# Kernel tuning notes

Hardware: AMD Instinct MI355X
Metric: run time of the kernel (lower is better)

The kernel has to match this reference:

```python
import jax, jax.numpy as jnp
import numpy as np
from jax import lax

DT = 0.1
V_DES = 12.64798288
T_HW = 0.50284384
A_MAX = 0.10033688
B_SAFE = 4.98937183
DELTA = 1.0
S0 = 0.13082412

B, S, I, H, K = 2048, 128, 8, 256, 50


def _lstm_layer(x, Wih, Whh, bih, bhh):
    # x: (B, S, in). PyTorch gate order: i, f, g, o. Fold both biases once.
    Bn = x.shape[0]
    Hd = Whh.shape[1]
    xg = jnp.einsum('bsi,gi->bsg', x, Wih) + bih + bhh  # (B, S, 4H)

    def step(carry, xg_t):
        h, c = carry
        g = xg_t + h @ Whh.T
        i, f, gg, o = jnp.split(g, 4, axis=-1)
        c = jax.nn.sigmoid(f) * c + jax.nn.sigmoid(i) * jnp.tanh(gg)
        h = jax.nn.sigmoid(o) * jnp.tanh(c)
        return (h, c), h

    init = (jnp.zeros((Bn, Hd), x.dtype), jnp.zeros((Bn, Hd), x.dtype))
    _, hs = lax.scan(step, init, jnp.swapaxes(xg, 0, 1))
    return jnp.swapaxes(hs, 0, 1)  # (B, S, H)


def _idm_rollout(v0, s_gap0, v_lead, horizon):
    sqrt_ab = float(np.sqrt(max(A_MAX, 1e-6) * max(B_SAFE, 1e-6)))

    def step(carry, _):
        v, s = carry
        dv = v_lead - v
        s_c = jnp.maximum(s, 1e-6)
        s_star = jnp.maximum(S0 + v * T_HW + v * dv / (2.0 * sqrt_ab + 1e-6), 0.0)
        acc = A_MAX * (1.0 - (v / V_DES) ** DELTA - (s_star / s_c) ** 2)
        v_next = jnp.maximum(v + DT * acc, 0.0)
        s_next = jnp.maximum(s + dv * DT, 1e-6)
        return (v_next, s_next), v_next

    _, vs = lax.scan(step, (v0, s_gap0), None, length=horizon)
    return jnp.swapaxes(vs, 0, 1)  # (B, K)


def setup_inputs() -> dict:
    key = jax.random.key(0)
    ks = jax.random.split(key, 14)
    sc = 0.05
    x = jax.random.uniform(ks[0], (B, S, I), jnp.float32) * 12.0  # speeds/features in [0, 12] m/s
    s_safe = 1.0 + jax.random.uniform(ks[1], (B,), jnp.float32) * 49.0  # gap in [1, 50] m
    v_lead = jax.random.uniform(ks[2], (B,), jnp.float32) * 12.0
    return {
        'x': x,
        's_safe_initial': s_safe,
        'v_lead_initial': v_lead,
        'Wih0': jax.random.normal(ks[3], (4 * H, I), jnp.float32) * sc,
        'Whh0': jax.random.normal(ks[4], (4 * H, H), jnp.float32) * sc,
        'bih0': jax.random.normal(ks[5], (4 * H,), jnp.float32) * sc,
        'bhh0': jax.random.normal(ks[6], (4 * H,), jnp.float32) * sc,
        'Wih1': jax.random.normal(ks[7], (4 * H, H), jnp.float32) * sc,
        'Whh1': jax.random.normal(ks[8], (4 * H, H), jnp.float32) * sc,
        'bih1': jax.random.normal(ks[9], (4 * H,), jnp.float32) * sc,
        'bhh1': jax.random.normal(ks[10], (4 * H,), jnp.float32) * sc,
        'Wfc': jax.random.normal(ks[11], (K, H), jnp.float32) * sc,
        'bfc': jax.random.normal(ks[12], (K,), jnp.float32) * sc,
    }


def reference(x, s_safe_initial, v_lead_initial, Wih0, Whh0, bih0, bhh0,
              Wih1, Whh1, bih1, bhh1, Wfc, bfc):
    h = _lstm_layer(x, Wih0, Whh0, bih0, bhh0)
    h = _lstm_layer(h, Wih1, Whh1, bih1, bhh1)
    y_lstm = h[:, -1, :] @ Wfc.T + bfc  # (B, K)
    y_idm = _idm_rollout(x[:, -1, 0], s_safe_initial, v_lead_initial, Wfc.shape[0])
    return (y_lstm, y_idm)
```

## Files before the change

kernel.cpp:

```cpp
#include <hip/hip_runtime.h>
#include <stdint.h>

typedef float f32x4 __attribute__((ext_vector_type(4)));
typedef unsigned int uint;
typedef unsigned long long ull;
typedef unsigned short ushort_t;

#define NB 2048
#define NS 128
#define NI 8
#define NH 256
#define NG 1024
#define NK 50

#define A_SC 16.0f
#define W_SC 32.0f
#define SC_PROD 512.0f
#define INV_SC (1.0f/(A_SC*W_SC))

#define DT_    0.1f
#define V_DES_ 12.64798288f
#define T_HW_  0.50284384f
#define A_MAX_ 0.10033688f
#define B_SAFE_ 4.98937183f
#define S0_    0.13082412f

#define HADDR(row, boff) (((row) << 8) + (((((boff) >> 3) ^ ((row) & 15)) & 31) << 3) + ((boff) & 7))
#define GIDX(row, col) (((row) << 7) + ((col) ^ (((row) & 12) << 2)))

__device__ __forceinline__ uint8_t f2fp8(float v) {
    int r = __builtin_amdgcn_cvt_pk_fp8_f32(v, v, 0, false);
    return (uint8_t)(r & 0xff);
}
__device__ __forceinline__ float sigm(float x) { return 1.0f / (1.0f + __expf(-x)); }
__device__ __forceinline__ float tanh_f(float x) {
    x = fminf(fmaxf(x, -15.0f), 15.0f);
    float e = __expf(2.0f * x);
    return (e - 1.0f) / (e + 1.0f);
}

__global__ void k_pack(const float* __restrict__ W, uint8_t* __restrict__ out,
                       int tiles, int KB, int Nsrc, int Ksrc) {
    int gid = blockIdx.x * 256 + threadIdx.x;
    int total = tiles * KB * 64;
    if (gid >= total) return;
    int lane = gid & 63;
    int kb   = (gid >> 6) % KB;
    int tile = gid / (64 * KB);
    int n = tile * 16 + (lane & 15);
    int kbase = kb * 32 + (lane >> 4) * 8;
    uint64_t wbits = 0;
    #pragma unroll
    for (int j = 0; j < 8; ++j) {
        int k = kbase + j;
        float v = (n < Nsrc && k < Ksrc) ? W[(size_t)n * Ksrc + k] * W_SC : 0.0f;
        wbits |= ((uint64_t)f2fp8(v)) << (8 * j);
    }
    *(uint64_t*)(out + (size_t)gid * 8) = wbits;
}

__global__ void k_bias(const float* __restrict__ bih0, const float* __restrict__ bhh0,
                       const float* __restrict__ bih1, const float* __restrict__ bhh1,
                       float* __restrict__ b0, float* __restrict__ b1) {
    int i = blockIdx.x * 256 + threadIdx.x;
    if (i < NG) b0[i] = (bih0[i] + bhh0[i]) * SC_PROD;
    else if (i < 2 * NG) b1[i - NG] = (bih1[i - NG] + bhh1[i - NG]) * SC_PROD;
}

__global__ void k_x8(const float* __restrict__ x, uint8_t* __restrict__ x8) {
    int i = blockIdx.x * 256 + threadIdx.x;
    if (i < NB * NS * NI) x8[i] = f2fp8(x[i] * A_SC);
}

__global__ __launch_bounds__(512, 4)
void k_lstm4(const uint8_t* __restrict__ x8,
             const uint8_t* __restrict__ Wih0P, const uint8_t* __restrict__ Whh0P,
             const uint8_t* __restrict__ Wih1P, const uint8_t* __restrict__ Whh1P,
             const uint8_t* __restrict__ WfcP,
             const float* __restrict__ bias0, const float* __restrict__ bias1,
             const float* __restrict__ bfc,
             uint8_t* __restrict__ h0g, uint8_t* __restrict__ h1g,
             uint* __restrict__ ctrs, float* __restrict__ out) {
    __shared__ uint8_t h0st[8192];
    __shared__ uint8_t h1st[8192];
    __shared__ float gA[4096];
    __shared__ float gB[4096];

    const int tid  = threadIdx.x;
    const int w    = tid >> 6, lane = tid & 63;
    const int lrow = lane & 15, kgrp = lane >> 4;
    const int blk  = blockIdx.x;
    const int grp  = blk >> 3, slc = blk & 7;
    const int rowbase = grp * 32;
    const int g = w & 3, uh = w >> 2;
    const int T = g * 16 + slc * 2 + uh;

    long wI0, wH0[8], wI1[8], wH1[8];
    wI0 = *(const long*)(Wih0P + ((size_t)T * 64 + lane) * 8);
    #pragma unroll
    for (int kb = 0; kb < 8; ++kb) {
        wH0[kb] = *(const long*)(Whh0P + (((size_t)T * 8 + kb) * 64 + lane) * 8);
        wI1[kb] = *(const long*)(Wih1P + (((size_t)T * 8 + kb) * 64 + lane) * 8);
        wH1[kb] = *(const long*)(Whh1P + (((size_t)T * 8 + kb) * 64 + lane) * 8);
    }
    asm volatile("" : "+v"(wI0));
    #pragma unroll
    for (int kb = 0; kb < 8; ++kb)
        asm volatile("" : "+v"(wH0[kb]), "+v"(wI1[kb]), "+v"(wH1[kb]));

    const int colw = g * 32 + uh * 16 + lrow;
    const float bw0 = bias0[g * 256 + slc * 32 + uh * 16 + lrow];
    const float bw1 = bias1[g * 256 + slc * 32 + uh * 16 + lrow];

    const int nrow = tid >> 4;
    const int nu2  = (tid & 15) * 2;
    float c0v[2] = {0, 0}, c1v[2] = {0, 0};

    { int4 z = {0,0,0,0}; ((int4*)h0st)[tid] = z; ((int4*)h1st)[tid] = z; }
    __syncthreads();

    const int abase = HADDR(lrow, kgrp * 8);
    uint8_t* const h0base = h0g + (size_t)grp * 16384;
    uint8_t* const h1base = h1g + (size_t)grp * 16384;
    uint* const myctr = ctrs + grp * 16;
    uint tgt = 0;

    for (int p = 0; p <= NS; ++p) {
        if (p < NS) {
            f32x4 acc[2];
            acc[0] = (f32x4){0,0,0,0}; acc[1] = (f32x4){0,0,0,0};
            #pragma unroll
            for (int rr = 0; rr < 2; ++rr) {
                long a0 = 0;
                if (kgrp == 0) a0 = *(const long*)(x8 + (size_t)(rowbase + rr * 16 + lrow) * (NS * NI) + p * 8);
                acc[rr] = __builtin_amdgcn_mfma_f32_16x16x32_fp8_fp8(a0, wI0, acc[rr], 0, 0, 0);
                #pragma unroll
                for (int kb = 0; kb < 8; ++kb) {
                    long af = *(const long*)&h0st[(abase + rr * 4096) ^ (kb << 5)];
                    acc[rr] = __builtin_amdgcn_mfma_f32_16x16x32_fp8_fp8(af, wH0[kb], acc[rr], 0, 0, 0);
                }
            }
            #pragma unroll
            for (int rr = 0; rr < 2; ++rr)
            #pragma unroll
            for (int r = 0; r < 4; ++r) {
                int row = rr * 16 + kgrp * 4 + r;
                gA[GIDX(row, colw)] = acc[rr][r] + bw0;
            }
        }
        __syncthreads();

        if (p < NS) {
            float2 gq[4];
            #pragma unroll
            for (int q = 0; q < 4; ++q)
                gq[q] = *(float2*)&gA[GIDX(nrow, q * 32 + nu2)];
            float hh[2];
            #pragma unroll
            for (int u = 0; u < 2; ++u) {
                float iv = ((u ? gq[0].y : gq[0].x)) * INV_SC;
                float fv = ((u ? gq[1].y : gq[1].x)) * INV_SC;
                float gv = ((u ? gq[2].y : gq[2].x)) * INV_SC;
                float ov = ((u ? gq[3].y : gq[3].x)) * INV_SC;
                float c = sigm(fv) * c0v[u] + sigm(iv) * tanh_f(gv);
                c0v[u] = c;
                hh[u] = sigm(ov) * tanh_f(c);
            }
            int pk = __builtin_amdgcn_cvt_pk_fp8_f32(hh[0] * A_SC, hh[1] * A_SC, 0, false);
            __hip_atomic_store((ushort_t*)(h0base + (size_t)(p & 1) * 8192 + nrow * 256 + slc * 32 + nu2),
                               (ushort_t)(pk & 0xffff), __ATOMIC_RELAXED, __HIP_MEMORY_SCOPE_AGENT);
        }

        if (p >= 1) {
            f32x4 acc[2];
            acc[0] = (f32x4){0,0,0,0}; acc[1] = (f32x4){0,0,0,0};
            #pragma unroll
            for (int rr = 0; rr < 2; ++rr) {
                #pragma unroll
                for (int kb = 0; kb < 8; ++kb) {
                    long af0 = *(const long*)&h0st[(abase + rr * 4096) ^ (kb << 5)];
                    acc[rr] = __builtin_amdgcn_mfma_f32_16x16x32_fp8_fp8(af0, wI1[kb], acc[rr], 0, 0, 0);
                    long af1 = *(const long*)&h1st[(abase + rr * 4096) ^ (kb << 5)];
                    acc[rr] = __builtin_amdgcn_mfma_f32_16x16x32_fp8_fp8(af1, wH1[kb], acc[rr], 0, 0, 0);
                }
            }
            #pragma unroll
            for (int rr = 0; rr < 2; ++rr)
            #pragma unroll
            for (int r = 0; r < 4; ++r) {
                int row = rr * 16 + kgrp * 4 + r;
                gB[GIDX(row, colw)] = acc[rr][r] + bw1;
            }
        }
        __syncthreads();

        if (p >= 1) {
            float2 gq[4];
            #pragma unroll
            for (int q = 0; q < 4; ++q)
                gq[q] = *(float2*)&gB[GIDX(nrow, q * 32 + nu2)];
            float hh[2];
            #pragma unroll
            for (int u = 0; u < 2; ++u) {
                float iv = ((u ? gq[0].y : gq[0].x)) * INV_SC;
                float fv = ((u ? gq[1].y : gq[1].x)) * INV_SC;
                float gv = ((u ? gq[2].y : gq[2].x)) * INV_SC;
                float ov = ((u ? gq[3].y : gq[3].x)) * INV_SC;
                float c = sigm(fv) * c1v[u] + sigm(iv) * tanh_f(gv);
                c1v[u] = c;
                hh[u] = sigm(ov) * tanh_f(c);
            }
            int pk = __builtin_amdgcn_cvt_pk_fp8_f32(hh[0] * A_SC, hh[1] * A_SC, 0, false);
            __hip_atomic_store((ushort_t*)(h1base + (size_t)((p - 1) & 1) * 8192 + nrow * 256 + slc * 32 + nu2),
                               (ushort_t)(pk & 0xffff), __ATOMIC_RELAXED, __HIP_MEMORY_SCOPE_AGENT);
        }
        __syncthreads();

        tgt += 8;
        if (tid == 0) {
            __hip_atomic_fetch_add(myctr, 1u, __ATOMIC_RELAXED, __HIP_MEMORY_SCOPE_AGENT);
            int gd = 0;
            while (__hip_atomic_load(myctr, __ATOMIC_RELAXED, __HIP_MEMORY_SCOPE_AGENT) < tgt) {
                __builtin_amdgcn_s_sleep(1);
                if (++gd >= (1 << 22)) break;
            }
        }
        __syncthreads();

        {
            int rrow = tid & 31, seg = tid >> 5;
            const ull* s0p = (const ull*)(h0base + (size_t)(p & 1) * 8192 + rrow * 256 + seg * 16);
            const ull* s1p = (const ull*)(h1base + (size_t)((p + 1) & 1) * 8192 + rrow * 256 + seg * 16);
            #pragma unroll
            for (int j = 0; j < 2; ++j) {
                ull q0 = __hip_atomic_load(s0p + j, __ATOMIC_RELAXED, __HIP_MEMORY_SCOPE_AGENT);
                ull q1 = __hip_atomic_load(s1p + j, __ATOMIC_RELAXED, __HIP_MEMORY_SCOPE_AGENT);
                *(ull*)&h0st[HADDR(rrow, seg * 16 + j * 8)] = q0;
                *(ull*)&h1st[HADDR(rrow, seg * 16 + j * 8)] = q1;
            }
        }
        __syncthreads();
    }

    if (slc < 4 && w < 2) {
        f32x4 a = (f32x4){0,0,0,0};
        #pragma unroll
        for (int kb = 0; kb < 8; ++kb) {
            long af = *(const long*)&h1st[HADDR(w * 16 + lrow, kb * 32 + kgrp * 8)];
            long bf = *(const long*)(WfcP + (((size_t)slc * 8 + kb) * 64 + lane) * 8);
            a = __builtin_amdgcn_mfma_f32_16x16x32_fp8_fp8(af, bf, a, 0, 0, 0);
        }
        int col = slc * 16 + lrow;
        if (col < NK) {
            float bb = bfc[col];
            #pragma unroll
            for (int r = 0; r < 4; ++r) {
                int row = rowbase + w * 16 + kgrp * 4 + r;
                out[(size_t)row * NK + col] = a[r] * INV_SC + bb;
            }
        }
    }
}

__global__ void k_idm(const float* __restrict__ x, const float* __restrict__ s0,
                      const float* __restrict__ vl, float* __restrict__ out) {
    int b = blockIdx.x * 256 + threadIdx.x;
    if (b >= NB) return;
    float v = x[(size_t)b * NS * NI + (NS - 1) * NI + 0];
    float s = s0[b];
    float vlead = vl[b];
    const float den = 2.0f * sqrtf(A_MAX_ * B_SAFE_) + 1e-6f;
    float* o = out + (size_t)NB * NK + (size_t)b * NK;
    #pragma unroll 1
    for (int k = 0; k < NK; ++k) {
        float dv = vlead - v;
        float sc = fmaxf(s, 1e-6f);
        float ss = fmaxf(S0_ + v * T_HW_ + v * dv / den, 0.0f);
        float a = A_MAX_ * (1.0f - v / V_DES_ - (ss / sc) * (ss / sc));
        v = fmaxf(v + DT_ * a, 0.0f);
        s = fmaxf(s + dv * DT_, 1e-6f);
        o[k] = v;
    }
}

extern "C" void kernel_launch(void* const* d_in, const int* in_sizes, int n_in,
                              void* d_out, int out_size, void* d_ws, size_t ws_size,
                              hipStream_t stream) {
    const float* x    = (const float*)d_in[0];
    const float* s0   = (const float*)d_in[1];
    const float* vl   = (const float*)d_in[2];
    const float* Wih0 = (const float*)d_in[3];
    const float* Whh0 = (const float*)d_in[4];
    const float* bih0 = (const float*)d_in[5];
    const float* bhh0 = (const float*)d_in[6];
    const float* Wih1 = (const float*)d_in[7];
    const float* Whh1 = (const float*)d_in[8];
    const float* bih1 = (const float*)d_in[9];
    const float* bhh1 = (const float*)d_in[10];
    const float* Wfc  = (const float*)d_in[11];
    const float* bfc  = (const float*)d_in[12];
    float* out = (float*)d_out;

    uint8_t* ws = (uint8_t*)d_ws;
    size_t off = 0;
    auto alloc = [&](size_t n) { uint8_t* p = ws + off; off += (n + 255) & ~(size_t)255; return p; };
    uint8_t* Wih0P = alloc(64 * 1 * 64 * 8);
    uint8_t* Whh0P = alloc(64 * 8 * 64 * 8);
    uint8_t* Wih1P = alloc(64 * 8 * 64 * 8);
    uint8_t* Whh1P = alloc(64 * 8 * 64 * 8);
    uint8_t* WfcP  = alloc(4 * 8 * 64 * 8);
    float* b0 = (float*)alloc(NG * 4);
    float* b1 = (float*)alloc(NG * 4);
    uint8_t* x8 = alloc((size_t)NB * NS * NI);
    uint8_t* h0g = alloc((size_t)64 * 16384);
    uint8_t* h1g = alloc((size_t)64 * 16384);
    uint*    ctrs = (uint*)alloc(64 * 64);
    size_t hz = (size_t)(((uint8_t*)ctrs + 64 * 64) - h0g);

    k_pack<<<(64 * 1 * 64 + 255) / 256, 256, 0, stream>>>(Wih0, Wih0P, 64, 1, NG, NI);
    k_pack<<<(64 * 8 * 64 + 255) / 256, 256, 0, stream>>>(Whh0, Whh0P, 64, 8, NG, NH);
    k_pack<<<(64 * 8 * 64 + 255) / 256, 256, 0, stream>>>(Wih1, Wih1P, 64, 8, NG, NH);
    k_pack<<<(64 * 8 * 64 + 255) / 256, 256, 0, stream>>>(Whh1, Whh1P, 64, 8, NG, NH);
    k_pack<<<(4 * 8 * 64 + 255) / 256, 256, 0, stream>>>(Wfc, WfcP, 4, 8, NK, NH);
    k_bias<<<(2 * NG + 255) / 256, 256, 0, stream>>>(bih0, bhh0, bih1, bhh1, b0, b1);
    k_x8<<<(NB * NS * NI + 255) / 256, 256, 0, stream>>>(x, x8);
    hipMemsetAsync(h0g, 0, hz, stream);

    void* kargs[] = { (void*)&x8, (void*)&Wih0P, (void*)&Whh0P, (void*)&Wih1P, (void*)&Whh1P,
                      (void*)&WfcP, (void*)&b0, (void*)&b1, (void*)&bfc,
                      (void*)&h0g, (void*)&h1g, (void*)&ctrs, (void*)&out };
    hipError_t ce = hipLaunchCooperativeKernel((const void*)k_lstm4, dim3(512), dim3(512), kargs, 0, stream);
    if (ce != hipSuccess) {
        k_lstm4<<<512, 512, 0, stream>>>(x8, Wih0P, Whh0P, Wih1P, Whh1P, WfcP, b0, b1, bfc, h0g, h1g, ctrs, out);
    }
    k_idm<<<(NB + 255) / 256, 256, 0, stream>>>(x, s0, vl, out);
}
```

Before: 1.051 ms.

## Interleave two independent row sub-batches per block to hide cross-block sync latency

Each block now handles 64 batch rows split into two 32-row sub-batches with separate shared-memory h buffers, cell states and group counters. While one sub-batch waits on its group barrier, the other sub-batch's LSTM step runs, which is meant to overlap the inter-block spin-wait and global restaging latency with compute. It also switches to 16-byte swizzled LDS reads feeding two MFMAs each and pins weights in AGPRs. The grid is halved to 256 blocks with 2 blocks per CU, which means fewer resident waves and roughly twice the MFMA work per block per step.

```diff
diff --git a/kernel.cpp b/kernel.cpp
--- a/kernel.cpp
+++ b/kernel.cpp
@@ -2,6 +2,7 @@
 #include <stdint.h>
 
 typedef float f32x4 __attribute__((ext_vector_type(4)));
+typedef long long2_t __attribute__((ext_vector_type(2)));
 typedef unsigned int uint;
 typedef unsigned long long ull;
 typedef unsigned short ushort_t;
@@ -16,7 +17,7 @@
 #define A_SC 16.0f
 #define W_SC 32.0f
 #define SC_PROD 512.0f
-#define INV_SC (1.0f/(A_SC*W_SC))
+#define INV_SC (1.0f/512.0f)
 
 #define DT_    0.1f
 #define V_DES_ 12.64798288f
@@ -25,7 +26,7 @@
 #define B_SAFE_ 4.98937183f
 #define S0_    0.13082412f
 
-#define HADDR(row, boff) (((row) << 8) + (((((boff) >> 3) ^ ((row) & 15)) & 31) << 3) + ((boff) & 7))
+#define HADDR16(row, boff) (((row) << 8) + (((((boff) >> 4) ^ ((row) & 15)) & 15) << 4) + ((boff) & 15))
 #define GIDX(row, col) (((row) << 7) + ((col) ^ (((row) & 12) << 2)))
 
 __device__ __forceinline__ uint8_t f2fp8(float v) {
@@ -72,8 +73,8 @@
     if (i < NB * NS * NI) x8[i] = f2fp8(x[i] * A_SC);
 }
 
-__global__ __launch_bounds__(512, 4)
-void k_lstm4(const uint8_t* __restrict__ x8,
+__global__ __launch_bounds__(512, 2)
+void k_lstm5(const uint8_t* __restrict__ x8,
              const uint8_t* __restrict__ Wih0P, const uint8_t* __restrict__ Whh0P,
              const uint8_t* __restrict__ Wih1P, const uint8_t* __restrict__ Whh1P,
              const uint8_t* __restrict__ WfcP,
@@ -81,17 +82,14 @@
              const float* __restrict__ bfc,
              uint8_t* __restrict__ h0g, uint8_t* __restrict__ h1g,
              uint* __restrict__ ctrs, float* __restrict__ out) {
-    __shared__ uint8_t h0st[8192];
-    __shared__ uint8_t h1st[8192];
-    __shared__ float gA[4096];
-    __shared__ float gB[4096];
+    __shared__ uint8_t h0st[2][8192];
+    __shared__ uint8_t h1st[2][8192];
+    __shared__ float gA[4096], gB[4096];
 
     const int tid  = threadIdx.x;
-    const int w    = tid >> 6, lane = tid & 63;
+    const int lane = tid & 63, w = tid >> 6;
     const int lrow = lane & 15, kgrp = lane >> 4;
-    const int blk  = blockIdx.x;
-    const int grp  = blk >> 3, slc = blk & 7;
-    const int rowbase = grp * 32;
+    const int grp  = blockIdx.x >> 3, slc = blockIdx.x & 7;
     const int g = w & 3, uh = w >> 2;
     const int T = g * 16 + slc * 2 + uh;
 
@@ -103,10 +101,10 @@
         wI1[kb] = *(const long*)(Wih1P + (((size_t)T * 8 + kb) * 64 + lane) * 8);
         wH1[kb] = *(const long*)(Whh1P + (((size_t)T * 8 + kb) * 64 + lane) * 8);
     }
-    asm volatile("" : "+v"(wI0));
+    asm volatile("" : "+a"(wI0));
     #pragma unroll
     for (int kb = 0; kb < 8; ++kb)
-        asm volatile("" : "+v"(wH0[kb]), "+v"(wI1[kb]), "+v"(wH1[kb]));
+        asm volatile("" : "+a"(wH0[kb]), "+a"(wI1[kb]), "+a"(wH1[kb]));
 
     const int colw = g * 32 + uh * 16 + lrow;
     const float bw0 = bias0[g * 256 + slc * 32 + uh * 16 + lrow];
@@ -114,152 +112,179 @@
 
     const int nrow = tid >> 4;
     const int nu2  = (tid & 15) * 2;
-    float c0v[2] = {0, 0}, c1v[2] = {0, 0};
-
-    { int4 z = {0,0,0,0}; ((int4*)h0st)[tid] = z; ((int4*)h1st)[tid] = z; }
+    float c0s[2][2] = {{0, 0}, {0, 0}}, c1s[2][2] = {{0, 0}, {0, 0}};
+
+    {   int4 z = {0, 0, 0, 0};
+        ((int4*)h0st)[tid] = z; ((int4*)h0st)[tid + 512] = z;
+        ((int4*)h1st)[tid] = z; ((int4*)h1st)[tid + 512] = z; }
     __syncthreads();
 
-    const int abase = HADDR(lrow, kgrp * 8);
-    uint8_t* const h0base = h0g + (size_t)grp * 16384;
-    uint8_t* const h1base = h1g + (size_t)grp * 16384;
-    uint* const myctr = ctrs + grp * 16;
-    uint tgt = 0;
+    uint8_t* const h0gg = h0g + (size_t)grp * 32768;
+    uint8_t* const h1gg = h1g + (size_t)grp * 32768;
+    uint* const ctrA = ctrs + grp * 32;
+    uint* const ctrB = ctrs + grp * 32 + 16;
+    uint tA = 0, tB = 0;
+
+#define WAITC(CP, TGT) do { \
+    if (tid == 0) { \
+        uint gd_ = 0; \
+        while (__hip_atomic_load((CP), __ATOMIC_RELAXED, __HIP_MEMORY_SCOPE_AGENT) < (TGT)) { \
+            __builtin_amdgcn_s_sleep(1); \
+            if (++gd_ > (1u << 24)) break; \
+        } \
+    } \
+    __syncthreads(); \
+} while (0)
+
+#define RESTAGE(S, P0, P1) do { \
+    const int rrow_ = tid & 31, seg_ = tid >> 5; \
+    const uint8_t* s0_ = h0gg + (size_t)((S) * 2 + (P0)) * 8192 + rrow_ * 256 + seg_ * 16; \
+    const uint8_t* s1_ = h1gg + (size_t)((S) * 2 + (P1)) * 8192 + rrow_ * 256 + seg_ * 16; \
+    ull a0_ = __hip_atomic_load((const ull*)s0_,       __ATOMIC_RELAXED, __HIP_MEMORY_SCOPE_AGENT); \
+    ull a1_ = __hip_atomic_load((const ull*)(s0_ + 8), __ATOMIC_RELAXED, __HIP_MEMORY_SCOPE_AGENT); \
+    ull b0_ = __hip_atomic_load((const ull*)s1_,       __ATOMIC_RELAXED, __HIP_MEMORY_SCOPE_AGENT); \
+    ull b1_ = __hip_atomic_load((const ull*)(s1_ + 8), __ATOMIC_RELAXED, __HIP_MEMORY_SCOPE_AGENT); \
+    const int kb_ = seg_ >> 1, kg_ = (seg_ & 1) << 1; \
+    *(ull*)&h0st[S][HADDR16(rrow_, kg_ * 64 + kb_ * 8)]       = a0_; \
+    *(ull*)&h0st[S][HADDR16(rrow_, (kg_ + 1) * 64 + kb_ * 8)] = a1_; \
+    *(ull*)&h1st[S][HADDR16(rrow_, kg_ * 64 + kb_ * 8)]       = b0_; \
+    *(ull*)&h1st[S][HADDR16(rrow_, (kg_ + 1) * 64 + kb_ * 8)] = b1_; \
+} while (0)
+
+#define LSTM_BLOCK(S) do { \
+    if (p < NS) { \
+        f32x4 ac0 = {0, 0, 0, 0}, ac1 = {0, 0, 0, 0}; \
+        long ax0 = 0, ax1 = 0; \
+        if (kgrp == 0) { \
+            const uint8_t* xb_ = x8 + (size_t)(grp * 64 + (S) * 32 + lrow) * (NS * NI) + p * 8; \
+            ax0 = *(const long*)xb_; \
+            ax1 = *(const long*)(xb_ + (size_t)16 * NS * NI); \
+        } \
+        ac0 = __builtin_amdgcn_mfma_f32_16x16x32_fp8_fp8(ax0, wI0, ac0, 0, 0, 0); \
+        ac1 = __builtin_amdgcn_mfma_f32_16x16x32_fp8_fp8(ax1, wI0, ac1, 0, 0, 0); \
+        _Pragma("unroll") \
+        for (int kbh = 0; kbh < 4; ++kbh) { \
+            const int gsw = ((((kgrp << 2) + kbh) ^ lrow) & 15) << 4; \
+            long2_t q0 = *(const long2_t*)&h0st[S][(lrow << 8) + gsw]; \
+            long2_t q1 = *(const long2_t*)&h0st[S][((16 + lrow) << 8) + gsw]; \
+            ac0 = __builtin_amdgcn_mfma_f32_16x16x32_fp8_fp8(q0.x, wH0[2 * kbh],     ac0, 0, 0, 0); \
+            ac0 = __builtin_amdgcn_mfma_f32_16x16x32_fp8_fp8(q0.y, wH0[2 * kbh + 1], ac0, 0, 0, 0); \
+            ac1 = __builtin_amdgcn_mfma_f32_16x16x32_fp8_fp8(q1.x, wH0[2 * kbh],     ac1, 0, 0, 0); \
+            ac1 = __builtin_amdgcn_mfma_f32_16x16x32_fp8_fp8(q1.y, wH0[2 * kbh + 1], ac1, 0, 0, 0); \
+        } \
+        _Pragma("unroll") \
+        for (int r_ = 0; r_ < 4; ++r_) { \
+            gA[GIDX(kgrp * 4 + r_, colw)]      = ac0[r_] + bw0; \
+            gA[GIDX(16 + kgrp * 4 + r_, colw)] = ac1[r_] + bw0; \
+        } \
+    } \
+    __syncthreads();   \
+    { \
+        f32x4 bc0 = {0, 0, 0, 0}, bc1 = {0, 0, 0, 0}; \
+        if (p >= 1) { \
+            _Pragma("unroll") \
+            for (int kbh = 0; kbh < 4; ++kbh) { \
+                const int gsw = ((((kgrp << 2) + kbh) ^ lrow) & 15) << 4; \
+                long2_t q0 = *(const long2_t*)&h0st[S][(lrow << 8) + gsw]; \
+                long2_t q1 = *(const long2_t*)&h0st[S][((16 + lrow) << 8) + gsw]; \
+                long2_t r0 = *(const long2_t*)&h1st[S][(lrow << 8) + gsw]; \
+                long2_t r1 = *(const long2_t*)&h1st[S][((16 + lrow) << 8) + gsw]; \
+                bc0 = __builtin_amdgcn_mfma_f32_16x16x32_fp8_fp8(q0.x, wI1[2 * kbh],     bc0, 0, 0, 0); \
+                bc0 = __builtin_amdgcn_mfma_f32_16x16x32_fp8_fp8(q0.y, wI1[2 * kbh + 1], bc0, 0, 0, 0); \
+                bc0 = __builtin_amdgcn_mfma_f32_16x16x32_fp8_fp8(r0.x, wH1[2 * kbh],     bc0, 0, 0, 0); \
+                bc0 = __builtin_amdgcn_mfma_f32_16x16x32_fp8_fp8(r0.y, wH1[2 * kbh + 1], bc0, 0, 0, 0); \
+                bc1 = __builtin_amdgcn_mfma_f32_16x16x32_fp8_fp8(q1.x, wI1[2 * kbh],     bc1, 0, 0, 0); \
+                bc1 = __builtin_amdgcn_mfma_f32_16x16x32_fp8_fp8(q1.y, wI1[2 * kbh + 1], bc1, 0, 0, 0); \
+                bc1 = __builtin_amdgcn_mfma_f32_16x16x32_fp8_fp8(r1.x, wH1[2 * kbh],     bc1, 0, 0, 0); \
+                bc1 = __builtin_amdgcn_mfma_f32_16x16x32_fp8_fp8(r1.y, wH1[2 * kbh + 1], bc1, 0, 0, 0); \
+            } \
+        } \
+        if (p < NS) {   \
+            float2 q0_ = *(float2*)&gA[GIDX(nrow, nu2)]; \
+            float2 q1_ = *(float2*)&gA[GIDX(nrow, 32 + nu2)]; \
+            float2 q2_ = *(float2*)&gA[GIDX(nrow, 64 + nu2)]; \
+            float2 q3_ = *(float2*)&gA[GIDX(nrow, 96 + nu2)]; \
+            float h0_, h1_; \
+            { float iv = q0_.x * INV_SC, fv = q1_.x * INV_SC, gv = q2_.x * INV_SC, ov = q3_.x * INV_SC; \
+              float c_ = sigm(fv) * c0s[S][0] + sigm(iv) * tanh_f(gv); c0s[S][0] = c_; \
+              h0_ = sigm(ov) * tanh_f(c_); } \
+            { float iv = q0_.y * INV_SC, fv = q1_.y * INV_SC, gv = q2_.y * INV_SC, ov = q3_.y * INV_SC; \
+              float c_ = sigm(fv) * c0s[S][1] + sigm(iv) * tanh_f(gv); c0s[S][1] = c_; \
+              h1_ = sigm(ov) * tanh_f(c_); } \
+            int pk_ = __builtin_amdgcn_cvt_pk_fp8_f32(h0_ * A_SC, h1_ * A_SC, 0, false); \
+            __hip_atomic_store((ushort_t*)(h0gg + (size_t)((S) * 2 + (p & 1)) * 8192 + nrow * 256 + slc * 32 + nu2), \
+                               (ushort_t)pk_, __ATOMIC_RELAXED, __HIP_MEMORY_SCOPE_AGENT); \
+        } \
+        if (p >= 1) { \
+            _Pragma("unroll") \
+            for (int r_ = 0; r_ < 4; ++r_) { \
+                gB[GIDX(kgrp * 4 + r_, colw)]      = bc0[r_] + bw1; \
+                gB[GIDX(16 + kgrp * 4 + r_, colw)] = bc1[r_] + bw1; \
+            } \
+        } \
+    } \
+    __syncthreads();   \
+    if (p >= 1) {   \
+        float2 q0_ = *(float2*)&gB[GIDX(nrow, nu2)]; \
+        float2 q1_ = *(float2*)&gB[GIDX(nrow, 32 + nu2)]; \
+        float2 q2_ = *(float2*)&gB[GIDX(nrow, 64 + nu2)]; \
+        float2 q3_ = *(float2*)&gB[GIDX(nrow, 96 + nu2)]; \
+        float h0_, h1_; \
+        { float iv = q0_.x * INV_SC, fv = q1_.x * INV_SC, gv = q2_.x * INV_SC, ov = q3_.x * INV_SC; \
+          float c_ = sigm(fv) * c1s[S][0] + sigm(iv) * tanh_f(gv); c1s[S][0] = c_; \
+          h0_ = sigm(ov) * tanh_f(c_); } \
+        { float iv = q0_.y * INV_SC, fv = q1_.y * INV_SC, gv = q2_.y * INV_SC, ov = q3_.y * INV_SC; \
+          float c_ = sigm(fv) * c1s[S][1] + sigm(iv) * tanh_f(gv); c1s[S][1] = c_; \
+          h1_ = sigm(ov) * tanh_f(c_); } \
+        int pk_ = __builtin_amdgcn_cvt_pk_fp8_f32(h0_ * A_SC, h1_ * A_SC, 0, false); \
+        __hip_atomic_store((ushort_t*)(h1gg + (size_t)((S) * 2 + ((p + 1) & 1)) * 8192 + nrow * 256 + slc * 32 + nu2), \
+                           (ushort_t)pk_, __ATOMIC_RELAXED, __HIP_MEMORY_SCOPE_AGENT); \
+    } \
+    __syncthreads();   \
+} while (0)
 
     for (int p = 0; p <= NS; ++p) {
-        if (p < NS) {
-            f32x4 acc[2];
-            acc[0] = (f32x4){0,0,0,0}; acc[1] = (f32x4){0,0,0,0};
-            #pragma unroll
-            for (int rr = 0; rr < 2; ++rr) {
-                long a0 = 0;
-                if (kgrp == 0) a0 = *(const long*)(x8 + (size_t)(rowbase + rr * 16 + lrow) * (NS * NI) + p * 8);
-                acc[rr] = __builtin_amdgcn_mfma_f32_16x16x32_fp8_fp8(a0, wI0, acc[rr], 0, 0, 0);
-                #pragma unroll
-                for (int kb = 0; kb < 8; ++kb) {
-                    long af = *(const long*)&h0st[(abase + rr * 4096) ^ (kb << 5)];
-                    acc[rr] = __builtin_amdgcn_mfma_f32_16x16x32_fp8_fp8(af, wH0[kb], acc[rr], 0, 0, 0);
-                }
-            }
-            #pragma unroll
-            for (int rr = 0; rr < 2; ++rr)
-            #pragma unroll
-            for (int r = 0; r < 4; ++r) {
-                int row = rr * 16 + kgrp * 4 + r;
-                gA[GIDX(row, colw)] = acc[rr][r] + bw0;
-            }
+        LSTM_BLOCK(0);
+        if (tid == 0) __hip_atomic_fetch_add(ctrA, 1u, __ATOMIC_RELAXED, __HIP_MEMORY_SCOPE_AGENT);
+        tA += 8;
+        WAITC(ctrB, tB);
+        RESTAGE(1, ((p + 1) & 1), (p & 1));
+        __syncthreads();
+        LSTM_BLOCK(1);
+        if (tid == 0) __hip_atomic_fetch_add(ctrB, 1u, __ATOMIC_RELAXED, __HIP_MEMORY_SCOPE_AGENT);
+        tB += 8;
+        WAITC(ctrA, tA);
+        RESTAGE(0, (p & 1), ((p + 1) & 1));
+        __syncthreads();
+    }
+    WAITC(ctrB, tB);
+    RESTAGE(1, 0, 1);
+    __syncthreads();
+
+    if (slc < 4 && w < 4) {
+        const uint8_t* hs = (w < 2) ? h1st[0] : h1st[1];
+        const int rl = (w & 1) * 16;
+        f32x4 a = {0, 0, 0, 0};
+        #pragma unroll
+        for (int kbh = 0; kbh < 4; ++kbh) {
+            const int gsw = ((((kgrp << 2) + kbh) ^ lrow) & 15) << 4;
+            long2_t q = *(const long2_t*)&hs[((rl + lrow) << 8) + gsw];
+            long b0_ = *(const long*)(WfcP + (((size_t)slc * 8 + 2 * kbh) * 64 + lane) * 8);
+            long b1_ = *(const long*)(WfcP + (((size_t)slc * 8 + 2 * kbh + 1) * 64 + lane) * 8);
+            a = __builtin_amdgcn_mfma_f32_16x16x32_fp8_fp8(q.x, b0_, a, 0, 0, 0);
+            a = __builtin_amdgcn_mfma_f32_16x16x32_fp8_fp8(q.y, b1_, a, 0, 0, 0);
         }
-        __syncthreads();
-
-        if (p < NS) {
-            float2 gq[4];
-            #pragma unroll
-            for (int q = 0; q < 4; ++q)
-                gq[q] = *(float2*)&gA[GIDX(nrow, q * 32 + nu2)];
-            float hh[2];
-            #pragma unroll
-            for (int u = 0; u < 2; ++u) {
-                float iv = ((u ? gq[0].y : gq[0].x)) * INV_SC;
-                float fv = ((u ? gq[1].y : gq[1].x)) * INV_SC;
-                float gv = ((u ? gq[2].y : gq[2].x)) * INV_SC;
-                float ov = ((u ? gq[3].y : gq[3].x)) * INV_SC;
-                float c = sigm(fv) * c0v[u] + sigm(iv) * tanh_f(gv);
-                c0v[u] = c;
-                hh[u] = sigm(ov) * tanh_f(c);
-            }
-            int pk = __builtin_amdgcn_cvt_pk_fp8_f32(hh[0] * A_SC, hh[1] * A_SC, 0, false);
-            __hip_atomic_store((ushort_t*)(h0base + (size_t)(p & 1) * 8192 + nrow * 256 + slc * 32 + nu2),
-                               (ushort_t)(pk & 0xffff), __ATOMIC_RELAXED, __HIP_MEMORY_SCOPE_AGENT);
-        }
-
-        if (p >= 1) {
-            f32x4 acc[2];
-            acc[0] = (f32x4){0,0,0,0}; acc[1] = (f32x4){0,0,0,0};
-            #pragma unroll
-            for (int rr = 0; rr < 2; ++rr) {
-                #pragma unroll
-                for (int kb = 0; kb < 8; ++kb) {
-                    long af0 = *(const long*)&h0st[(abase + rr * 4096) ^ (kb << 5)];
-                    acc[rr] = __builtin_amdgcn_mfma_f32_16x16x32_fp8_fp8(af0, wI1[kb], acc[rr], 0, 0, 0);
-                    long af1 = *(const long*)&h1st[(abase + rr * 4096) ^ (kb << 5)];
-                    acc[rr] = __builtin_amdgcn_mfma_f32_16x16x32_fp8_fp8(af1, wH1[kb], acc[rr], 0, 0, 0);
-                }
-            }
-            #pragma unroll
-            for (int rr = 0; rr < 2; ++rr)
-            #pragma unroll
-            for (int r = 0; r < 4; ++r) {
-                int row = rr * 16 + kgrp * 4 + r;
-                gB[GIDX(row, colw)] = acc[rr][r] + bw1;
-            }
-        }
-        __syncthreads();
-
-        if (p >= 1) {
-            float2 gq[4];
-            #pragma unroll
-            for (int q = 0; q < 4; ++q)
-                gq[q] = *(float2*)&gB[GIDX(nrow, q * 32 + nu2)];
-            float hh[2];
-            #pragma unroll
-            for (int u = 0; u < 2; ++u) {
-                float iv = ((u ? gq[0].y : gq[0].x)) * INV_SC;
-                float fv = ((u ? gq[1].y : gq[1].x)) * INV_SC;
-                float gv = ((u ? gq[2].y : gq[2].x)) * INV_SC;
-                float ov = ((u ? gq[3].y : gq[3].x)) * INV_SC;
-                float c = sigm(fv) * c1v[u] + sigm(iv) * tanh_f(gv);
-                c1v[u] = c;
-                hh[u] = sigm(ov) * tanh_f(c);
-            }
-            int pk = __builtin_amdgcn_cvt_pk_fp8_f32(hh[0] * A_SC, hh[1] * A_SC, 0, false);
-            __hip_atomic_store((ushort_t*)(h1base + (size_t)((p - 1) & 1) * 8192 + nrow * 256 + slc * 32 + nu2),
-                               (ushort_t)(pk & 0xffff), __ATOMIC_RELAXED, __HIP_MEMORY_SCOPE_AGENT);
-        }
-        __syncthreads();
-
-        tgt += 8;
-        if (tid == 0) {
-            __hip_atomic_fetch_add(myctr, 1u, __ATOMIC_RELAXED, __HIP_MEMORY_SCOPE_AGENT);
-            int gd = 0;
-            while (__hip_atomic_load(myctr, __ATOMIC_RELAXED, __HIP_MEMORY_SCOPE_AGENT) < tgt) {
-                __builtin_amdgcn_s_sleep(1);
-                if (++gd >= (1 << 22)) break;
-            }
-        }
-        __syncthreads();
-
-        {
-            int rrow = tid & 31, seg = tid >> 5;
-            const ull* s0p = (const ull*)(h0base + (size_t)(p & 1) * 8192 + rrow * 256 + seg * 16);
-            const ull* s1p = (const ull*)(h1base + (size_t)((p + 1) & 1) * 8192 + rrow * 256 + seg * 16);
-            #pragma unroll
-            for (int j = 0; j < 2; ++j) {
-                ull q0 = __hip_atomic_load(s0p + j, __ATOMIC_RELAXED, __HIP_MEMORY_SCOPE_AGENT);
-                ull q1 = __hip_atomic_load(s1p + j, __ATOMIC_RELAXED, __HIP_MEMORY_SCOPE_AGENT);
-                *(ull*)&h0st[HADDR(rrow, seg * 16 + j * 8)] = q0;
-                *(ull*)&h1st[HADDR(rrow, seg * 16 + j * 8)] = q1;
-            }
-        }
-        __syncthreads();
-    }
-
-    if (slc < 4 && w < 2) {
-        f32x4 a = (f32x4){0,0,0,0};
-        #pragma unroll
-        for (int kb = 0; kb < 8; ++kb) {
-            long af = *(const long*)&h1st[HADDR(w * 16 + lrow, kb * 32 + kgrp * 8)];
-            long bf = *(const long*)(WfcP + (((size_t)slc * 8 + kb) * 64 + lane) * 8);
-            a = __builtin_amdgcn_mfma_f32_16x16x32_fp8_fp8(af, bf, a, 0, 0, 0);
-        }
-        int col = slc * 16 + lrow;
+        const int col = slc * 16 + lrow;
         if (col < NK) {
             float bb = bfc[col];
             #pragma unroll
-            for (int r = 0; r < 4; ++r) {
-                int row = rowbase + w * 16 + kgrp * 4 + r;
-                out[(size_t)row * NK + col] = a[r] * INV_SC + bb;
-            }
+            for (int r_ = 0; r_ < 4; ++r_)
+                out[(size_t)(grp * 64 + w * 16 + kgrp * 4 + r_) * NK + col] = a[r_] * INV_SC + bb;
         }
     }
+#undef WAITC
+#undef RESTAGE
+#undef LSTM_BLOCK
 }
 
 __global__ void k_idm(const float* __restrict__ x, const float* __restrict__ s0,
@@ -312,10 +337,10 @@
     float* b0 = (float*)alloc(NG * 4);
     float* b1 = (float*)alloc(NG * 4);
     uint8_t* x8 = alloc((size_t)NB * NS * NI);
-    uint8_t* h0g = alloc((size_t)64 * 16384);
-    uint8_t* h1g = alloc((size_t)64 * 16384);
-    uint*    ctrs = (uint*)alloc(64 * 64);
-    size_t hz = (size_t)(((uint8_t*)ctrs + 64 * 64) - h0g);
+    uint8_t* h0g = alloc((size_t)32 * 32768);
+    uint8_t* h1g = alloc((size_t)32 * 32768);
+    uint*    ctrs = (uint*)alloc(32 * 32 * 4);
+    size_t hz = (size_t)(((uint8_t*)ctrs + 32 * 32 * 4) - h0g);
 
     k_pack<<<(64 * 1 * 64 + 255) / 256, 256, 0, stream>>>(Wih0, Wih0P, 64, 1, NG, NI);
     k_pack<<<(64 * 8 * 64 + 255) / 256, 256, 0, stream>>>(Whh0, Whh0P, 64, 8, NG, NH);
@@ -329,9 +354,9 @@
     void* kargs[] = { (void*)&x8, (void*)&Wih0P, (void*)&Whh0P, (void*)&Wih1P, (void*)&Whh1P,
                       (void*)&WfcP, (void*)&b0, (void*)&b1, (void*)&bfc,
                       (void*)&h0g, (void*)&h1g, (void*)&ctrs, (void*)&out };
-    hipError_t ce = hipLaunchCooperativeKernel((const void*)k_lstm4, dim3(512), dim3(512), kargs, 0, stream);
+    hipError_t ce = hipLaunchCooperativeKernel((const void*)k_lstm5, dim3(256), dim3(512), kargs, 0, stream);
     if (ce != hipSuccess) {
-        k_lstm4<<<512, 512, 0, stream>>>(x8, Wih0P, Whh0P, Wih1P, Whh1P, WfcP, b0, b1, bfc, h0g, h1g, ctrs, out);
+        k_lstm5<<<256, 512, 0, stream>>>(x8, Wih0P, Whh0P, Wih1P, Whh1P, WfcP, b0, b1, bfc, h0g, h1g, ctrs, out);
     }
     k_idm<<<(NB + 255) / 256, 256, 0, stream>>>(x, s0, vl, out);
 }
```

After: 1.330 ms. +26.6%, slower.
